# Kernel tuning notes

Hardware: AMD Instinct MI355X
Metric: run time of the kernel (lower is better)

Reference implementation:

```python
import jax, jax.numpy as jnp
import numpy as np

N = 50000   # nodes
E = 800000  # edges (before self-loops)
IN, HID, OUT = 128, 128, 64


def gcn_norm(edge_index, num_nodes):
    # add self loops with weight 1, then symmetric deg^-1/2 normalization
    loop = jnp.arange(num_nodes, dtype=edge_index.dtype)
    row = jnp.concatenate([edge_index[0], loop])
    col = jnp.concatenate([edge_index[1], loop])
    ew = jnp.ones(row.shape[0], dtype=jnp.float32)
    deg = jax.ops.segment_sum(ew, col, num_segments=num_nodes)
    dis = jnp.where(deg > 0, jax.lax.rsqrt(deg), 0.0)
    norm = dis[row] * ew * dis[col]
    return row, col, norm


def gcn_conv(x, row, col, norm, W, b):
    h = x @ W                                   # [N, F_out] dense GEMM
    msg = h[row] * norm[:, None]                # gather + scale over edges
    out = jax.ops.segment_sum(msg, col, num_segments=x.shape[0])  # scatter-add
    return out + b


def setup_inputs() -> dict:
    key = jax.random.key(0)
    k0, k1, k2, k3, k4, k5 = jax.random.split(key, 6)
    x = jax.random.normal(k0, (N, IN), dtype=jnp.float32)
    edge_index = jax.random.randint(k1, (2, E), 0, N, dtype=jnp.int32)
    # glorot-style init for linear weights, zeros for bias (PyG default)
    W1 = jax.random.normal(k2, (IN, HID), dtype=jnp.float32) * np.float32(np.sqrt(1.0 / IN))
    b1 = jnp.zeros((HID,), dtype=jnp.float32)
    W2 = jax.random.normal(k3, (HID, OUT), dtype=jnp.float32) * np.float32(np.sqrt(1.0 / HID))
    b2 = jnp.zeros((OUT,), dtype=jnp.float32)
    return {"x": x, "edge_index": edge_index, "W1": W1, "b1": b1, "W2": W2, "b2": b2}


def reference(x, edge_index, W1, b1, W2, b2):
    row, col, norm = gcn_norm(edge_index, x.shape[0])
    h = jax.nn.relu(gcn_conv(x, row, col, norm, W1, b1))
    # dropout is a no-op in eval mode (training=False)
    out = gcn_conv(h, row, col, norm, W2, b2)
    return out
```

## Files before the change

kernel.cpp:

```cpp
#include <hip/hip_runtime.h>
#include <hip/hip_fp16.h>


#define Nn 50000
#define Ne 800000
#define SCAN_B ((Nn + 1023) / 1024)

using f16x8 = _Float16 __attribute__((ext_vector_type(8)));
using f32x4 = float __attribute__((ext_vector_type(4)));

__global__ __launch_bounds__(256) void k_count(const int2* __restrict__ col2,
                                               int* __restrict__ degi,
                                               ushort2* __restrict__ rank2) {
  int t = blockIdx.x * 256 + threadIdx.x;
  if (t < Ne / 2) {
    int2 c = col2[t];
    unsigned short r0 = (unsigned short)atomicAdd(&degi[c.x], 1);
    unsigned short r1 = (unsigned short)atomicAdd(&degi[c.y], 1);
    ushort2 rk; rk.x = r0; rk.y = r1;
    rank2[t] = rk;
  }
}

__global__ __launch_bounds__(1024) void k_scan1(const int* __restrict__ degi,
                                                int* __restrict__ rowptr,
                                                float* __restrict__ dis,
                                                int* __restrict__ bsum) {
  __shared__ int wsum[16];
  int tid = threadIdx.x;
  int lane = tid & 63, wid = tid >> 6;
  int i = blockIdx.x * 1024 + tid;
  int v = (i < Nn) ? degi[i] : 0;
  if (i < Nn) dis[i] = rsqrtf((float)(v + 1));
  int incl = v;
  #pragma unroll
  for (int off = 1; off < 64; off <<= 1) {
    int t = __shfl_up(incl, off);
    if (lane >= off) incl += t;
  }
  if (lane == 63) wsum[wid] = incl;
  __syncthreads();
  if (wid == 0) {
    int wv = (lane < 16) ? wsum[lane] : 0;
    #pragma unroll
    for (int off = 1; off < 16; off <<= 1) {
      int t = __shfl_up(wv, off);
      if (lane >= off) wv += t;
    }
    if (lane < 16) wsum[lane] = wv;
  }
  __syncthreads();
  int woff = (wid > 0) ? wsum[wid - 1] : 0;
  if (i < Nn) rowptr[i] = woff + incl - v;
  if (tid == 0) bsum[blockIdx.x] = wsum[15];
}

__global__ __launch_bounds__(1024) void k_scan3(int* __restrict__ rowptr,
                                                const int* __restrict__ bsum) {
  __shared__ int off_s;
  int tid = threadIdx.x;
  if (tid < 64) {
    int v = (tid < SCAN_B) ? bsum[tid] : 0;
    int incl = v;
    #pragma unroll
    for (int off = 1; off < 64; off <<= 1) {
      int t = __shfl_up(incl, off);
      if (tid >= off) incl += t;
    }
    if (tid == (int)blockIdx.x) off_s = incl - v;
    if (blockIdx.x == 0 && tid == SCAN_B - 1) rowptr[Nn] = incl;
  }
  __syncthreads();
  int i = blockIdx.x * 1024 + tid;
  if (i < Nn) rowptr[i] += off_s;
}

__global__ __launch_bounds__(256) void k_fill(const int2* __restrict__ row2,
                                              const int2* __restrict__ col2,
                                              const int* __restrict__ rowptr,
                                              const ushort2* __restrict__ rank2,
                                              unsigned short* __restrict__ csr) {
  int t = blockIdx.x * 256 + threadIdx.x;
  if (t >= Ne / 2) return;
  int2 r = row2[t];
  int2 c = col2[t];
  ushort2 k = rank2[t];
  csr[rowptr[c.x] + (int)k.x] = (unsigned short)r.x;
  csr[rowptr[c.y] + (int)k.y] = (unsigned short)r.y;
}

template <int LDO>
__global__ __launch_bounds__(256) void k_gemm_mfma(const float* __restrict__ X,
                                                   const float* __restrict__ W,
                                                   __half* __restrict__ H, int n) {
  __shared__ _Float16 Xs[64 * 136];
  __shared__ _Float16 Wts[LDO * 136];
  const int tid = threadIdx.x;
  const int base = blockIdx.x * 64;

  {
    constexpr int C4 = LDO / 4;
    for (int idx4 = tid; idx4 < 32 * LDO; idx4 += 256) {
      int k = idx4 / C4;
      int c = (idx4 % C4) * 4;
      float4 wv = ((const float4*)W)[idx4];
      Wts[(c + 0) * 136 + k] = (_Float16)wv.x;
      Wts[(c + 1) * 136 + k] = (_Float16)wv.y;
      Wts[(c + 2) * 136 + k] = (_Float16)wv.z;
      Wts[(c + 3) * 136 + k] = (_Float16)wv.w;
    }
  }
  {
    for (int u = tid; u < 64 * 16; u += 256) {
      int r = u >> 4, seg = u & 15;
      int node = base + r;
      if (node >= n) node = n - 1;
      const float4* xg = (const float4*)(X + (size_t)node * 128 + seg * 8);
      float4 x0 = xg[0], x1 = xg[1];
      f16x8 hv;
      hv[0] = (_Float16)x0.x; hv[1] = (_Float16)x0.y;
      hv[2] = (_Float16)x0.z; hv[3] = (_Float16)x0.w;
      hv[4] = (_Float16)x1.x; hv[5] = (_Float16)x1.y;
      hv[6] = (_Float16)x1.z; hv[7] = (_Float16)x1.w;
      *(f16x8*)&Xs[r * 136 + seg * 8] = hv;
    }
  }
  __syncthreads();

  const int w = tid >> 6, lane = tid & 63;
  const int quad = lane >> 4, mrow = lane & 15;
  constexpr int NCT = LDO / 16;

  f32x4 acc[NCT];
  #pragma unroll
  for (int ct = 0; ct < NCT; ++ct) acc[ct] = (f32x4){0.f, 0.f, 0.f, 0.f};

  #pragma unroll
  for (int ko = 0; ko < 4; ++ko) {
    f16x8 av = *(const f16x8*)&Xs[(w * 16 + mrow) * 136 + ko * 32 + quad * 8];
    #pragma unroll
    for (int ct = 0; ct < NCT; ++ct) {
      f16x8 bv = *(const f16x8*)&Wts[(ct * 16 + mrow) * 136 + ko * 32 + quad * 8];
      acc[ct] = __builtin_amdgcn_mfma_f32_16x16x32_f16(av, bv, acc[ct], 0, 0, 0);
    }
  }

  #pragma unroll
  for (int ct = 0; ct < NCT; ++ct) {
    #pragma unroll
    for (int r = 0; r < 4; ++r) {
      int node = base + w * 16 + quad * 4 + r;
      if (node < n)
        H[(size_t)node * LDO + ct * 16 + mrow] = __float2half(acc[ct][r]);
    }
  }
}

__device__ __forceinline__ float2 h2f(unsigned int u) {
  return __half22float2(*(const __half2*)&u);
}

__global__ __launch_bounds__(256) void k_agg128_gemm64(
    const __half* __restrict__ H, const unsigned short* __restrict__ csr,
    const int* __restrict__ rowptr, const float* __restrict__ dis,
    const float* __restrict__ bias, const float* __restrict__ W2,
    __half* __restrict__ H2, int n) {
  __shared__ _Float16 Wts[64 * 136];
  __shared__ _Float16 Hs[16 * 136];

  const int tid = threadIdx.x;
  const int wid = tid >> 6, lane = tid & 63;
  const int sub = lane >> 4, fl = lane & 15;
  const int nb = wid * 4 + sub;
  const int v = blockIdx.x * 16 + nb;

  for (int idx4 = tid; idx4 < 2048; idx4 += 256) {
    int k = idx4 >> 4;
    int c = (idx4 & 15) * 4;
    float4 wv = ((const float4*)W2)[idx4];
    Wts[(c + 0) * 136 + k] = (_Float16)wv.x;
    Wts[(c + 1) * 136 + k] = (_Float16)wv.y;
    Wts[(c + 2) * 136 + k] = (_Float16)wv.z;
    Wts[(c + 3) * 136 + k] = (_Float16)wv.w;
  }

  int s = rowptr[v], e = rowptr[v + 1];
  float d = dis[v];
  float sw = d * d;
  const uint4* Hq = (const uint4*)H;
  uint4 hv = Hq[(size_t)v * 16 + fl];
  float2 p0 = h2f(hv.x), p1 = h2f(hv.y), p2 = h2f(hv.z), p3 = h2f(hv.w);
  float a0 = p0.x * sw, a1 = p0.y * sw, a2 = p1.x * sw, a3 = p1.y * sw;
  float a4 = p2.x * sw, a5 = p2.y * sw, a6 = p3.x * sw, a7 = p3.y * sw;
  constexpr int D = 6;
  int i = s;
  for (; i + D <= e; i += D) {
    int srcs[D];
    uint4 q[D];
    float wd[D];
    #pragma unroll
    for (int j = 0; j < D; ++j) srcs[j] = csr[i + j];
    #pragma unroll
    for (int j = 0; j < D; ++j) q[j] = Hq[(size_t)srcs[j] * 16 + fl];
    #pragma unroll
    for (int j = 0; j < D; ++j) wd[j] = dis[srcs[j]];
    #pragma unroll
    for (int j = 0; j < D; ++j) {
      float w = wd[j] * d;
      float2 t;
      t = h2f(q[j].x); a0 = fmaf(w, t.x, a0); a1 = fmaf(w, t.y, a1);
      t = h2f(q[j].y); a2 = fmaf(w, t.x, a2); a3 = fmaf(w, t.y, a3);
      t = h2f(q[j].z); a4 = fmaf(w, t.x, a4); a5 = fmaf(w, t.y, a5);
      t = h2f(q[j].w); a6 = fmaf(w, t.x, a6); a7 = fmaf(w, t.y, a7);
    }
  }
  if (i < e) {
    int srcs[D];
    uint4 q[D];
    float wd[D];
    #pragma unroll
    for (int j = 0; j < D; ++j) {
      int idx = (i + j < e) ? i + j : e - 1;
      srcs[j] = csr[idx];
    }
    #pragma unroll
    for (int j = 0; j < D; ++j) q[j] = Hq[(size_t)srcs[j] * 16 + fl];
    #pragma unroll
    for (int j = 0; j < D; ++j) wd[j] = dis[srcs[j]];
    #pragma unroll
    for (int j = 0; j < D; ++j) {
      float w = (i + j < e) ? wd[j] * d : 0.f;
      float2 t;
      t = h2f(q[j].x); a0 = fmaf(w, t.x, a0); a1 = fmaf(w, t.y, a1);
      t = h2f(q[j].y); a2 = fmaf(w, t.x, a2); a3 = fmaf(w, t.y, a3);
      t = h2f(q[j].z); a4 = fmaf(w, t.x, a4); a5 = fmaf(w, t.y, a5);
      t = h2f(q[j].w); a6 = fmaf(w, t.x, a6); a7 = fmaf(w, t.y, a7);
    }
  }
  {
    const float4* Bq = (const float4*)bias;
    float4 b0 = Bq[fl * 2], b1v = Bq[fl * 2 + 1];
    f16x8 hrow;
    hrow[0] = (_Float16)fmaxf(a0 + b0.x, 0.f);
    hrow[1] = (_Float16)fmaxf(a1 + b0.y, 0.f);
    hrow[2] = (_Float16)fmaxf(a2 + b0.z, 0.f);
    hrow[3] = (_Float16)fmaxf(a3 + b0.w, 0.f);
    hrow[4] = (_Float16)fmaxf(a4 + b1v.x, 0.f);
    hrow[5] = (_Float16)fmaxf(a5 + b1v.y, 0.f);
    hrow[6] = (_Float16)fmaxf(a6 + b1v.z, 0.f);
    hrow[7] = (_Float16)fmaxf(a7 + b1v.w, 0.f);
    *(f16x8*)&Hs[nb * 136 + fl * 8] = hrow;
  }
  __syncthreads();

  const int quad = lane >> 4, mrow = lane & 15;
  f32x4 acc = (f32x4){0.f, 0.f, 0.f, 0.f};
  #pragma unroll
  for (int ko = 0; ko < 4; ++ko) {
    f16x8 av = *(const f16x8*)&Hs[mrow * 136 + ko * 32 + quad * 8];
    f16x8 bv = *(const f16x8*)&Wts[(wid * 16 + mrow) * 136 + ko * 32 + quad * 8];
    acc = __builtin_amdgcn_mfma_f32_16x16x32_f16(av, bv, acc, 0, 0, 0);
  }
  #pragma unroll
  for (int r = 0; r < 4; ++r) {
    int node = blockIdx.x * 16 + quad * 4 + r;
    if (node < n)
      H2[(size_t)node * 64 + wid * 16 + mrow] = __float2half(acc[r]);
  }
}

__global__ __launch_bounds__(256) void k_agg64(const __half* __restrict__ H,
                                               const unsigned short* __restrict__ csr,
                                               const int* __restrict__ rowptr,
                                               const float* __restrict__ dis,
                                               const float* __restrict__ bias,
                                               float* __restrict__ Out, int n) {
  const int wid = threadIdx.x >> 6, lane = threadIdx.x & 63;
  const int sub = lane >> 4, fl = lane & 15;
  int v = blockIdx.x * 16 + wid * 4 + sub;
  if (v >= n) return;
  int s = rowptr[v], e = rowptr[v + 1];
  float d = dis[v];
  float sw = d * d;
  const uint2* Hq = (const uint2*)H;
  uint2 hv = Hq[(size_t)v * 16 + fl];
  float2 p0 = h2f(hv.x), p1 = h2f(hv.y);
  float a0 = p0.x * sw, a1 = p0.y * sw, a2 = p1.x * sw, a3 = p1.y * sw;
  constexpr int D = 8;
  int i = s;
  for (; i + D <= e; i += D) {
    int srcs[D];
    uint2 q[D];
    float wd[D];
    #pragma unroll
    for (int j = 0; j < D; ++j) srcs[j] = csr[i + j];
    #pragma unroll
    for (int j = 0; j < D; ++j) q[j] = Hq[(size_t)srcs[j] * 16 + fl];
    #pragma unroll
    for (int j = 0; j < D; ++j) wd[j] = dis[srcs[j]];
    #pragma unroll
    for (int j = 0; j < D; ++j) {
      float w = wd[j] * d;
      float2 t;
      t = h2f(q[j].x); a0 = fmaf(w, t.x, a0); a1 = fmaf(w, t.y, a1);
      t = h2f(q[j].y); a2 = fmaf(w, t.x, a2); a3 = fmaf(w, t.y, a3);
    }
  }
  if (i < e) {
    int srcs[D];
    uint2 q[D];
    float wd[D];
    #pragma unroll
    for (int j = 0; j < D; ++j) {
      int idx = (i + j < e) ? i + j : e - 1;
      srcs[j] = csr[idx];
    }
    #pragma unroll
    for (int j = 0; j < D; ++j) q[j] = Hq[(size_t)srcs[j] * 16 + fl];
    #pragma unroll
    for (int j = 0; j < D; ++j) wd[j] = dis[srcs[j]];
    #pragma unroll
    for (int j = 0; j < D; ++j) {
      float w = (i + j < e) ? wd[j] * d : 0.f;
      float2 t;
      t = h2f(q[j].x); a0 = fmaf(w, t.x, a0); a1 = fmaf(w, t.y, a1);
      t = h2f(q[j].y); a2 = fmaf(w, t.x, a2); a3 = fmaf(w, t.y, a3);
    }
  }
  const float4* Bq = (const float4*)bias;
  float4 b = Bq[fl];
  float4 o = make_float4(a0 + b.x, a1 + b.y, a2 + b.z, a3 + b.w);
  ((float4*)(Out + (size_t)v * 64))[fl] = o;
}

extern "C" void kernel_launch(void* const* d_in, const int* in_sizes, int n_in,
                              void* d_out, int out_size, void* d_ws, size_t ws_size,
                              hipStream_t stream) {
  const float* x  = (const float*)d_in[0];
  const int*   ei = (const int*)d_in[1];
  const int*   row = ei;
  const int*   col = ei + Ne;
  const float* W1 = (const float*)d_in[2];
  const float* b1 = (const float*)d_in[3];
  const float* W2 = (const float*)d_in[4];
  const float* b2 = (const float*)d_in[5];
  float* out = (float*)d_out;

  char* ws = (char*)d_ws;
  size_t off = 0;
  auto alloc = [&](size_t bytes) -> void* {
    void* p = ws + off;
    off += (bytes + 255) & ~(size_t)255;
    return p;
  };
  int*    degi   = (int*)   alloc(Nn * sizeof(int));
  int*    rowptr = (int*)   alloc((Nn + 1) * sizeof(int));
  float*  dis    = (float*) alloc(Nn * sizeof(float));
  int*    bsum   = (int*)   alloc(64 * sizeof(int));
  unsigned short* rank = (unsigned short*)alloc((size_t)Ne * sizeof(unsigned short));
  unsigned short* csr  = (unsigned short*)alloc((size_t)Ne * sizeof(unsigned short));
  __half* H1     = (__half*)alloc((size_t)Nn * 128 * sizeof(__half));
  __half* H2     = (__half*)alloc((size_t)Nn * 64 * sizeof(__half));

  hipMemsetAsync(degi, 0, Nn * sizeof(int), stream);

  const int E2B = (Ne / 2 + 255) / 256;
  const int NGB = (Nn + 15) / 16;
  const int GT  = (Nn + 63) / 64;

  k_count<<<E2B, 256, 0, stream>>>((const int2*)col, degi, (ushort2*)rank);
  k_scan1<<<SCAN_B, 1024, 0, stream>>>(degi, rowptr, dis, bsum);
  k_scan3<<<SCAN_B, 1024, 0, stream>>>(rowptr, bsum);
  k_fill<<<E2B, 256, 0, stream>>>((const int2*)row, (const int2*)col, rowptr,
                                  (const ushort2*)rank, csr);

  k_gemm_mfma<128><<<GT, 256, 0, stream>>>(x, W1, H1, Nn);
  k_agg128_gemm64<<<NGB, 256, 0, stream>>>(H1, csr, rowptr, dis, b1, W2, H2, Nn);
  k_agg64<<<NGB, 256, 0, stream>>>(H2, csr, rowptr, dis, b2, out, Nn);
}
```

Measured before the change: 206.5 us.

## Merge GEMM1 with degree count, precompute fp16 W2, prefetch CSR indices in aggregation

Runs the first dense GEMM and the edge degree-count atomics in one launch by splitting the grid, so the two independent stages overlap and one launch goes away. W2 is converted and transposed to fp16 once inside the scan kernel, and the aggregation blocks then copy it with vector loads instead of redoing the conversion per block. The aggregation loops are restructured to prefetch the next batch of CSR neighbour indices while the current gathers are in flight, with masked tails in place of a separate remainder path. The GEMM blocks reserve large shared memory, which the light count blocks also carry, and that may limit how many blocks reside at once.

```diff
diff --git a/kernel.cpp b/kernel.cpp
--- a/kernel.cpp
+++ b/kernel.cpp
@@ -5,20 +5,87 @@
 #define Nn 50000
 #define Ne 800000
 #define SCAN_B ((Nn + 1023) / 1024)
+#define GT ((Nn + 63) / 64)
+#define E2B ((Ne / 2 + 255) / 256)
 
 using f16x8 = _Float16 __attribute__((ext_vector_type(8)));
 using f32x4 = float __attribute__((ext_vector_type(4)));
 
-__global__ __launch_bounds__(256) void k_count(const int2* __restrict__ col2,
-                                               int* __restrict__ degi,
-                                               ushort2* __restrict__ rank2) {
-  int t = blockIdx.x * 256 + threadIdx.x;
-  if (t < Ne / 2) {
-    int2 c = col2[t];
-    unsigned short r0 = (unsigned short)atomicAdd(&degi[c.x], 1);
-    unsigned short r1 = (unsigned short)atomicAdd(&degi[c.y], 1);
-    ushort2 rk; rk.x = r0; rk.y = r1;
-    rank2[t] = rk;
+__global__ __launch_bounds__(256) void k_gemm128_count(
+    const float* __restrict__ X, const float* __restrict__ W,
+    __half* __restrict__ H, const int2* __restrict__ col2,
+    int* __restrict__ degi, ushort2* __restrict__ rank2) {
+  __shared__ _Float16 Xs[64 * 136];
+  __shared__ _Float16 Wts[128 * 136];
+
+  if ((int)blockIdx.x >= GT) {
+    int t = ((int)blockIdx.x - GT) * 256 + threadIdx.x;
+    if (t < Ne / 2) {
+      int2 c = col2[t];
+      unsigned short r0 = (unsigned short)atomicAdd(&degi[c.x], 1);
+      unsigned short r1 = (unsigned short)atomicAdd(&degi[c.y], 1);
+      ushort2 rk; rk.x = r0; rk.y = r1;
+      rank2[t] = rk;
+    }
+    return;
+  }
+
+  const int tid = threadIdx.x;
+  const int base = blockIdx.x * 64;
+
+  {
+    for (int idx4 = tid; idx4 < 32 * 128; idx4 += 256) {
+      int k = idx4 >> 5;
+      int c = (idx4 & 31) * 4;
+      float4 wv = ((const float4*)W)[idx4];
+      Wts[(c + 0) * 136 + k] = (_Float16)wv.x;
+      Wts[(c + 1) * 136 + k] = (_Float16)wv.y;
+      Wts[(c + 2) * 136 + k] = (_Float16)wv.z;
+      Wts[(c + 3) * 136 + k] = (_Float16)wv.w;
+    }
+  }
+  {
+    for (int u = tid; u < 64 * 16; u += 256) {
+      int r = u >> 4, seg = u & 15;
+      int node = base + r;
+      if (node >= Nn) node = Nn - 1;
+      const float4* xg = (const float4*)(X + (size_t)node * 128 + seg * 8);
+      float4 x0 = xg[0], x1 = xg[1];
+      f16x8 hv;
+      hv[0] = (_Float16)x0.x; hv[1] = (_Float16)x0.y;
+      hv[2] = (_Float16)x0.z; hv[3] = (_Float16)x0.w;
+      hv[4] = (_Float16)x1.x; hv[5] = (_Float16)x1.y;
+      hv[6] = (_Float16)x1.z; hv[7] = (_Float16)x1.w;
+      *(f16x8*)&Xs[r * 136 + seg * 8] = hv;
+    }
+  }
+  __syncthreads();
+
+  const int w = tid >> 6, lane = tid & 63;
+  const int quad = lane >> 4, mrow = lane & 15;
+
+  f32x4 acc[8];
+  #pragma unroll
+  for (int ct = 0; ct < 8; ++ct) acc[ct] = (f32x4){0.f, 0.f, 0.f, 0.f};
+
+  #pragma unroll
+  for (int ko = 0; ko < 4; ++ko) {
+    f16x8 av = *(const f16x8*)&Xs[(w * 16 + mrow) * 136 + ko * 32 + quad * 8];
+    #pragma unroll
+    for (int ct = 0; ct < 8; ++ct) {
+      f16x8 bv = *(const f16x8*)&Wts[(ct * 16 + mrow) * 136 + ko * 32 + quad * 8];
+      acc[ct] = __builtin_amdgcn_mfma_f32_16x16x32_f16(av, bv, acc[ct], 0, 0, 0);
+    }
+  }
+
+  #pragma unroll
+  for (int ct = 0; ct < 8; ++ct) {
+    #pragma unroll
+    for (int r = 0; r < 4; ++r) {
+      int node = base + w * 16 + quad * 4 + r;
+      if (node < Nn)
+        H[(size_t)node * 128 + ct * 16 + mrow] = __float2half(acc[ct][r]);
+    }
   }
 }
 
@@ -56,7 +123,9 @@
 }
 
 __global__ __launch_bounds__(1024) void k_scan3(int* __restrict__ rowptr,
-                                                const int* __restrict__ bsum) {
+                                                const int* __restrict__ bsum,
+                                                const float* __restrict__ W2,
+                                                _Float16* __restrict__ W2h) {
   __shared__ int off_s;
   int tid = threadIdx.x;
   if (tid < 64) {
@@ -73,6 +142,17 @@
   __syncthreads();
   int i = blockIdx.x * 1024 + tid;
   if (i < Nn) rowptr[i] += off_s;
+  if (blockIdx.x == 1) {
+    for (int idx4 = tid; idx4 < 2048; idx4 += 1024) {
+      int k = idx4 >> 4;
+      int c = (idx4 & 15) * 4;
+      float4 wv = ((const float4*)W2)[idx4];
+      W2h[(c + 0) * 128 + k] = (_Float16)wv.x;
+      W2h[(c + 1) * 128 + k] = (_Float16)wv.y;
+      W2h[(c + 2) * 128 + k] = (_Float16)wv.z;
+      W2h[(c + 3) * 128 + k] = (_Float16)wv.w;
+    }
+  }
 }
 
 __global__ __launch_bounds__(256) void k_fill(const int2* __restrict__ row2,
@@ -89,73 +169,6 @@
   csr[rowptr[c.y] + (int)k.y] = (unsigned short)r.y;
 }
 
-template <int LDO>
-__global__ __launch_bounds__(256) void k_gemm_mfma(const float* __restrict__ X,
-                                                   const float* __restrict__ W,
-                                                   __half* __restrict__ H, int n) {
-  __shared__ _Float16 Xs[64 * 136];
-  __shared__ _Float16 Wts[LDO * 136];
-  const int tid = threadIdx.x;
-  const int base = blockIdx.x * 64;
-
-  {
-    constexpr int C4 = LDO / 4;
-    for (int idx4 = tid; idx4 < 32 * LDO; idx4 += 256) {
-      int k = idx4 / C4;
-      int c = (idx4 % C4) * 4;
-      float4 wv = ((const float4*)W)[idx4];
-      Wts[(c + 0) * 136 + k] = (_Float16)wv.x;
-      Wts[(c + 1) * 136 + k] = (_Float16)wv.y;
-      Wts[(c + 2) * 136 + k] = (_Float16)wv.z;
-      Wts[(c + 3) * 136 + k] = (_Float16)wv.w;
-    }
-  }
-  {
-    for (int u = tid; u < 64 * 16; u += 256) {
-      int r = u >> 4, seg = u & 15;
-      int node = base + r;
-      if (node >= n) node = n - 1;
-      const float4* xg = (const float4*)(X + (size_t)node * 128 + seg * 8);
-      float4 x0 = xg[0], x1 = xg[1];
-      f16x8 hv;
-      hv[0] = (_Float16)x0.x; hv[1] = (_Float16)x0.y;
-      hv[2] = (_Float16)x0.z; hv[3] = (_Float16)x0.w;
-      hv[4] = (_Float16)x1.x; hv[5] = (_Float16)x1.y;
-      hv[6] = (_Float16)x1.z; hv[7] = (_Float16)x1.w;
-      *(f16x8*)&Xs[r * 136 + seg * 8] = hv;
-    }
-  }
-  __syncthreads();
-
-  const int w = tid >> 6, lane = tid & 63;
-  const int quad = lane >> 4, mrow = lane & 15;
-  constexpr int NCT = LDO / 16;
-
-  f32x4 acc[NCT];
-  #pragma unroll
-  for (int ct = 0; ct < NCT; ++ct) acc[ct] = (f32x4){0.f, 0.f, 0.f, 0.f};
-
-  #pragma unroll
-  for (int ko = 0; ko < 4; ++ko) {
-    f16x8 av = *(const f16x8*)&Xs[(w * 16 + mrow) * 136 + ko * 32 + quad * 8];
-    #pragma unroll
-    for (int ct = 0; ct < NCT; ++ct) {
-      f16x8 bv = *(const f16x8*)&Wts[(ct * 16 + mrow) * 136 + ko * 32 + quad * 8];
-      acc[ct] = __builtin_amdgcn_mfma_f32_16x16x32_f16(av, bv, acc[ct], 0, 0, 0);
-    }
-  }
-
-  #pragma unroll
-  for (int ct = 0; ct < NCT; ++ct) {
-    #pragma unroll
-    for (int r = 0; r < 4; ++r) {
-      int node = base + w * 16 + quad * 4 + r;
-      if (node < n)
-        H[(size_t)node * LDO + ct * 16 + mrow] = __float2half(acc[ct][r]);
-    }
-  }
-}
-
 __device__ __forceinline__ float2 h2f(unsigned int u) {
   return __half22float2(*(const __half2*)&u);
 }
@@ -163,7 +176,7 @@
 __global__ __launch_bounds__(256) void k_agg128_gemm64(
     const __half* __restrict__ H, const unsigned short* __restrict__ csr,
     const int* __restrict__ rowptr, const float* __restrict__ dis,
-    const float* __restrict__ bias, const float* __restrict__ W2,
+    const float* __restrict__ bias, const _Float16* __restrict__ W2h,
     __half* __restrict__ H2, int n) {
   __shared__ _Float16 Wts[64 * 136];
   __shared__ _Float16 Hs[16 * 136];
@@ -174,14 +187,12 @@
   const int nb = wid * 4 + sub;
   const int v = blockIdx.x * 16 + nb;
 
-  for (int idx4 = tid; idx4 < 2048; idx4 += 256) {
-    int k = idx4 >> 4;
-    int c = (idx4 & 15) * 4;
-    float4 wv = ((const float4*)W2)[idx4];
-    Wts[(c + 0) * 136 + k] = (_Float16)wv.x;
-    Wts[(c + 1) * 136 + k] = (_Float16)wv.y;
-    Wts[(c + 2) * 136 + k] = (_Float16)wv.z;
-    Wts[(c + 3) * 136 + k] = (_Float16)wv.w;
+  {
+    const f16x8* Wq = (const f16x8*)W2h;
+    for (int u = tid; u < 1024; u += 256) {
+      int c = u >> 4, k8 = u & 15;
+      *(f16x8*)&Wts[c * 136 + k8 * 8] = Wq[u];
+    }
   }
 
   int s = rowptr[v], e = rowptr[v + 1];
@@ -193,48 +204,37 @@
   float a0 = p0.x * sw, a1 = p0.y * sw, a2 = p1.x * sw, a3 = p1.y * sw;
   float a4 = p2.x * sw, a5 = p2.y * sw, a6 = p3.x * sw, a7 = p3.y * sw;
   constexpr int D = 6;
-  int i = s;
-  for (; i + D <= e; i += D) {
+  if (s < e) {
     int srcs[D];
-    uint4 q[D];
-    float wd[D];
-    #pragma unroll
-    for (int j = 0; j < D; ++j) srcs[j] = csr[i + j];
-    #pragma unroll
-    for (int j = 0; j < D; ++j) q[j] = Hq[(size_t)srcs[j] * 16 + fl];
-    #pragma unroll
-    for (int j = 0; j < D; ++j) wd[j] = dis[srcs[j]];
     #pragma unroll
     for (int j = 0; j < D; ++j) {
-      float w = wd[j] * d;
-      float2 t;
-      t = h2f(q[j].x); a0 = fmaf(w, t.x, a0); a1 = fmaf(w, t.y, a1);
-      t = h2f(q[j].y); a2 = fmaf(w, t.x, a2); a3 = fmaf(w, t.y, a3);
-      t = h2f(q[j].z); a4 = fmaf(w, t.x, a4); a5 = fmaf(w, t.y, a5);
-      t = h2f(q[j].w); a6 = fmaf(w, t.x, a6); a7 = fmaf(w, t.y, a7);
-    }
-  }
-  if (i < e) {
-    int srcs[D];
-    uint4 q[D];
-    float wd[D];
-    #pragma unroll
-    for (int j = 0; j < D; ++j) {
-      int idx = (i + j < e) ? i + j : e - 1;
-      srcs[j] = csr[idx];
-    }
-    #pragma unroll
-    for (int j = 0; j < D; ++j) q[j] = Hq[(size_t)srcs[j] * 16 + fl];
-    #pragma unroll
-    for (int j = 0; j < D; ++j) wd[j] = dis[srcs[j]];
-    #pragma unroll
-    for (int j = 0; j < D; ++j) {
-      float w = (i + j < e) ? wd[j] * d : 0.f;
-      float2 t;
-      t = h2f(q[j].x); a0 = fmaf(w, t.x, a0); a1 = fmaf(w, t.y, a1);
-      t = h2f(q[j].y); a2 = fmaf(w, t.x, a2); a3 = fmaf(w, t.y, a3);
-      t = h2f(q[j].z); a4 = fmaf(w, t.x, a4); a5 = fmaf(w, t.y, a5);
-      t = h2f(q[j].w); a6 = fmaf(w, t.x, a6); a7 = fmaf(w, t.y, a7);
+      int idx = s + j;
+      srcs[j] = csr[(idx < e) ? idx : (e - 1)];
+    }
+    for (int base = s; base < e; base += D) {
+      uint4 q[D];
+      float wd[D];
+      #pragma unroll
+      for (int j = 0; j < D; ++j) q[j] = Hq[(size_t)srcs[j] * 16 + fl];
+      #pragma unroll
+      for (int j = 0; j < D; ++j) wd[j] = dis[srcs[j]];
+      int ns[D];
+      #pragma unroll
+      for (int j = 0; j < D; ++j) {
+        int idx = base + D + j;
+        ns[j] = csr[(idx < e) ? idx : (e - 1)];
+      }
+      #pragma unroll
+      for (int j = 0; j < D; ++j) {
+        float w = ((base + j) < e) ? wd[j] * d : 0.f;
+        float2 t;
+        t = h2f(q[j].x); a0 = fmaf(w, t.x, a0); a1 = fmaf(w, t.y, a1);
+        t = h2f(q[j].y); a2 = fmaf(w, t.x, a2); a3 = fmaf(w, t.y, a3);
+        t = h2f(q[j].z); a4 = fmaf(w, t.x, a4); a5 = fmaf(w, t.y, a5);
+        t = h2f(q[j].w); a6 = fmaf(w, t.x, a6); a7 = fmaf(w, t.y, a7);
+      }
+      #pragma unroll
+      for (int j = 0; j < D; ++j) srcs[j] = ns[j];
     }
   }
   {
@@ -287,44 +287,35 @@
   float2 p0 = h2f(hv.x), p1 = h2f(hv.y);
   float a0 = p0.x * sw, a1 = p0.y * sw, a2 = p1.x * sw, a3 = p1.y * sw;
   constexpr int D = 8;
-  int i = s;
-  for (; i + D <= e; i += D) {
+  if (s < e) {
     int srcs[D];
-    uint2 q[D];
-    float wd[D];
-    #pragma unroll
-    for (int j = 0; j < D; ++j) srcs[j] = csr[i + j];
-    #pragma unroll
-    for (int j = 0; j < D; ++j) q[j] = Hq[(size_t)srcs[j] * 16 + fl];
-    #pragma unroll
-    for (int j = 0; j < D; ++j) wd[j] = dis[srcs[j]];
     #pragma unroll
     for (int j = 0; j < D; ++j) {
-      float w = wd[j] * d;
-      float2 t;
-      t = h2f(q[j].x); a0 = fmaf(w, t.x, a0); a1 = fmaf(w, t.y, a1);
-      t = h2f(q[j].y); a2 = fmaf(w, t.x, a2); a3 = fmaf(w, t.y, a3);
-    }
-  }
-  if (i < e) {
-    int srcs[D];
-    uint2 q[D];
-    float wd[D];
-    #pragma unroll
-    for (int j = 0; j < D; ++j) {
-      int idx = (i + j < e) ? i + j : e - 1;
-      srcs[j] = csr[idx];
-    }
-    #pragma unroll
-    for (int j = 0; j < D; ++j) q[j] = Hq[(size_t)srcs[j] * 16 + fl];
-    #pragma unroll
-    for (int j = 0; j < D; ++j) wd[j] = dis[srcs[j]];
-    #pragma unroll
-    for (int j = 0; j < D; ++j) {
-      float w = (i + j < e) ? wd[j] * d : 0.f;
-      float2 t;
-      t = h2f(q[j].x); a0 = fmaf(w, t.x, a0); a1 = fmaf(w, t.y, a1);
-      t = h2f(q[j].y); a2 = fmaf(w, t.x, a2); a3 = fmaf(w, t.y, a3);
+      int idx = s + j;
+      srcs[j] = csr[(idx < e) ? idx : (e - 1)];
+    }
+    for (int base = s; base < e; base += D) {
+      uint2 q[D];
+      float wd[D];
+      #pragma unroll
+      for (int j = 0; j < D; ++j) q[j] = Hq[(size_t)srcs[j] * 16 + fl];
+      #pragma unroll
+      for (int j = 0; j < D; ++j) wd[j] = dis[srcs[j]];
+      int ns[D];
+      #pragma unroll
+      for (int j = 0; j < D; ++j) {
+        int idx = base + D + j;
+        ns[j] = csr[(idx < e) ? idx : (e - 1)];
+      }
+      #pragma unroll
+      for (int j = 0; j < D; ++j) {
+        float w = ((base + j) < e) ? wd[j] * d : 0.f;
+        float2 t;
+        t = h2f(q[j].x); a0 = fmaf(w, t.x, a0); a1 = fmaf(w, t.y, a1);
+        t = h2f(q[j].y); a2 = fmaf(w, t.x, a2); a3 = fmaf(w, t.y, a3);
+      }
+      #pragma unroll
+      for (int j = 0; j < D; ++j) srcs[j] = ns[j];
     }
   }
   const float4* Bq = (const float4*)bias;
@@ -361,20 +352,18 @@
   unsigned short* csr  = (unsigned short*)alloc((size_t)Ne * sizeof(unsigned short));
   __half* H1     = (__half*)alloc((size_t)Nn * 128 * sizeof(__half));
   __half* H2     = (__half*)alloc((size_t)Nn * 64 * sizeof(__half));
+  _Float16* W2h  = (_Float16*)alloc(64 * 128 * sizeof(_Float16));
 
   hipMemsetAsync(degi, 0, Nn * sizeof(int), stream);
 
-  const int E2B = (Ne / 2 + 255) / 256;
   const int NGB = (Nn + 15) / 16;
-  const int GT  = (Nn + 63) / 64;
-
-  k_count<<<E2B, 256, 0, stream>>>((const int2*)col, degi, (ushort2*)rank);
+
+  k_gemm128_count<<<GT + E2B, 256, 0, stream>>>(x, W1, H1, (const int2*)col,
+                                                degi, (ushort2*)rank);
   k_scan1<<<SCAN_B, 1024, 0, stream>>>(degi, rowptr, dis, bsum);
-  k_scan3<<<SCAN_B, 1024, 0, stream>>>(rowptr, bsum);
+  k_scan3<<<SCAN_B, 1024, 0, stream>>>(rowptr, bsum, W2, W2h);
   k_fill<<<E2B, 256, 0, stream>>>((const int2*)row, (const int2*)col, rowptr,
                                   (const ushort2*)rank, csr);
-
-  k_gemm_mfma<128><<<GT, 256, 0, stream>>>(x, W1, H1, Nn);
-  k_agg128_gemm64<<<NGB, 256, 0, stream>>>(H1, csr, rowptr, dis, b1, W2, H2, Nn);
+  k_agg128_gemm64<<<NGB, 256, 0, stream>>>(H1, csr, rowptr, dis, b1, W2h, H2, Nn);
   k_agg64<<<NGB, 256, 0, stream>>>(H2, csr, rowptr, dis, b2, out, Nn);
 }
```

Measured after the change: 196.2 us. 1.05x faster.
